# Kernel optimization log

Measured on AMD Instinct MI355X. Metric: run time of the kernel, lower is better.

The kernel has to match this reference:

```python
import jax, jax.numpy as jnp
import numpy as np

NT, NC = 100000, 25000
ETT, ECT = 800000, 400000
DIN_T, DIN_C = 64, 32
H, C = 4, 32
HID = H * C  # 128
SLOPE = 0.2  # GATConv LeakyReLU negative slope


def setup_inputs() -> dict:
    key = jax.random.key(0)
    ks = jax.random.split(key, 24)
    def p(i, shape, s=0.05):
        return jax.random.normal(ks[i], shape, dtype=jnp.float32) * s
    return {
        'x_target': jax.random.normal(ks[0], (NT, DIN_T), dtype=jnp.float32),
        'x_context': jax.random.normal(ks[1], (NC, DIN_C), dtype=jnp.float32),
        'edge_tt': jax.random.randint(ks[2], (2, ETT), 0, NT),
        'edge_ct_src': jax.random.randint(ks[3], (ECT,), 0, NC),
        'edge_ct_dst': jax.random.randint(ks[4], (ECT,), 0, NT),
        'W_pre_t': p(5, (DIN_T, HID)), 'b_pre_t': jnp.zeros((HID,), jnp.float32),
        'W_pre_c': p(6, (DIN_C, HID)), 'b_pre_c': jnp.zeros((HID,), jnp.float32),
        'W_sd': p(7, (HID, HID)), 'att_src_sd': p(8, (H, C)), 'att_dst_sd': p(9, (H, C)), 'b_sd': jnp.zeros((HID,), jnp.float32),
        'W_ds': p(10, (HID, HID)), 'att_src_ds': p(11, (H, C)), 'att_dst_ds': p(12, (H, C)), 'b_ds': jnp.zeros((HID,), jnp.float32),
        'W_ct_src': p(13, (HID, HID)), 'W_ct_dst': p(14, (HID, HID)), 'att_src_ct': p(15, (H, C)), 'att_dst_ct': p(16, (H, C)), 'b_ct': jnp.zeros((HID,), jnp.float32),
        'W_out': p(17, (HID, HID)), 'b_out': jnp.zeros((HID,), jnp.float32),
    }


def _gat(h_src, h_dst, att_s, att_d, src, dst, n_dst, bias):
    # h_src: [N_src,H,C] transformed src feats; h_dst: [N_dst,H,C]
    a_s = jnp.einsum('nhc,hc->nh', h_src, att_s)  # [N_src,H]
    a_d = jnp.einsum('nhc,hc->nh', h_dst, att_d)  # [N_dst,H]
    e = a_s[src] + a_d[dst]                        # [E,H]
    e = jnp.where(e > 0, e, SLOPE * e)             # LeakyReLU(0.2)
    m = jax.ops.segment_max(e, dst, num_segments=n_dst)  # stable softmax per dst
    ex = jnp.exp(e - m[dst])
    den = jax.ops.segment_sum(ex, dst, num_segments=n_dst)
    alpha = ex / den[dst]                          # [E,H]
    msg = h_src[src] * alpha[:, :, None]           # [E,H,C]
    out = jax.ops.segment_sum(msg, dst, num_segments=n_dst)
    return out.reshape(n_dst, H * C) + bias


def reference(x_target, x_context, edge_tt, edge_ct_src, edge_ct_dst,
              W_pre_t, b_pre_t, W_pre_c, b_pre_c,
              W_sd, att_src_sd, att_dst_sd, b_sd,
              W_ds, att_src_ds, att_dst_ds, b_ds,
              W_ct_src, W_ct_dst, att_src_ct, att_dst_ct, b_ct,
              W_out, b_out):
    # HeteroDictLinear pretransform + relu
    h_t = jax.nn.relu(x_target @ W_pre_t + b_pre_t)   # [NT,128]
    h_c = jax.nn.relu(x_context @ W_pre_c + b_pre_c)  # [NC,128]
    res = h_t
    # DirGATConv on (target,to,target): forward + reversed, each w/ self-loops
    loops = jnp.arange(NT)
    src_f = jnp.concatenate([edge_tt[0], loops]); dst_f = jnp.concatenate([edge_tt[1], loops])
    src_r = jnp.concatenate([edge_tt[1], loops]); dst_r = jnp.concatenate([edge_tt[0], loops])
    hs = (h_t @ W_sd).reshape(NT, H, C)
    out_sd = _gat(hs, hs, att_src_sd, att_dst_sd, src_f, dst_f, NT, b_sd)
    hd = (h_t @ W_ds).reshape(NT, H, C)
    out_ds = _gat(hd, hd, att_src_ds, att_dst_ds, src_r, dst_r, NT, b_ds)
    out_tt = 0.5 * out_sd + 0.5 * out_ds  # (1-alpha), alpha with alpha=0.5
    # bipartite GATConv on (context,to,target), no self loops
    hcs = (h_c @ W_ct_src).reshape(NC, H, C)
    htd = (h_t @ W_ct_dst).reshape(NT, H, C)
    out_ct = _gat(hcs, htd, att_src_ct, att_dst_ct, edge_ct_src, edge_ct_dst, NT, b_ct)
    # HeteroConv aggr='mean' over the two edge types hitting 'target'
    x = 0.5 * (out_tt + out_ct)
    x = jax.nn.relu(x + res)  # skip connection + relu
    return x @ W_out + b_out
```

## Files before the change

kernel.cpp:

```cpp
#include <hip/hip_runtime.h>
#include <cstdint>
#include <cstddef>

typedef unsigned short u16;
typedef unsigned int u32;

#define NT 100000
#define NC 25000
#define ETT 800000
#define ECT 400000
#define SLOPE 0.2f
#define OFFS (NT + 4)

#define NBK 782
#define NBLK 256
#define CHT ((ETT + NBLK - 1) / NBLK)
#define CHC ((ECT + NBLK - 1) / NBLK)
#define TOTC (3 * NBK * NBLK)
#define NSB ((TOTC + 2047) / 2048)

typedef __attribute__((ext_vector_type(8))) short bf16x8;
typedef __attribute__((ext_vector_type(4))) float f32x4;

__device__ __forceinline__ u16 f2bf(float f) {
  u32 u = __float_as_uint(f);
  u32 r = (u >> 16) & 1u;
  return (u16)((u + 0x7fffu + r) >> 16);
}
__device__ __forceinline__ float lof(u32 p) { return __uint_as_float(p << 16); }
__device__ __forceinline__ float hif(u32 p) { return __uint_as_float(p & 0xffff0000u); }

__global__ __launch_bounds__(256) void pre_t_kernel(const float* __restrict__ in,
    const float* __restrict__ W, const float* __restrict__ bias,
    const float* __restrict__ fold_cd, u16* __restrict__ h_t,
    float* __restrict__ aD, int N)
{
  __shared__ float s_in[32][33];
  __shared__ float s_W[32][128];
  __shared__ float s_fold[512];
  const int t = threadIdx.x;
  s_fold[t] = fold_cd[t];
  s_fold[t + 256] = fold_cd[t + 256];
  const int row0 = blockIdx.x * 32;
  const int rl = t >> 3, cg = t & 7;
  const int gr = row0 + rl;
  float acc[4][4];
  for (int g = 0; g < 4; ++g)
    for (int j = 0; j < 4; ++j)
      acc[g][j] = bias[g * 32 + cg * 4 + j];
  for (int kc = 0; kc < 64; kc += 32) {
    {
      float4 f = make_float4(0.f, 0.f, 0.f, 0.f);
      if (gr < N) f = *(const float4*)(in + (size_t)gr * 64 + kc + cg * 4);
      s_in[rl][cg * 4 + 0] = f.x; s_in[rl][cg * 4 + 1] = f.y;
      s_in[rl][cg * 4 + 2] = f.z; s_in[rl][cg * 4 + 3] = f.w;
    }
    for (int j = 0; j < 4; ++j) {
      const int idx = t + j * 256;
      const int k = idx >> 5, c4 = (idx & 31) * 4;
      *(float4*)&s_W[k][c4] = *(const float4*)(W + (size_t)(kc + k) * 128 + c4);
    }
    __syncthreads();
#pragma unroll 8
    for (int k = 0; k < 32; ++k) {
      const float a = s_in[rl][k];
      for (int g = 0; g < 4; ++g) {
        const float4 w = *(const float4*)&s_W[k][g * 32 + cg * 4];
        acc[g][0] = fmaf(a, w.x, acc[g][0]);
        acc[g][1] = fmaf(a, w.y, acc[g][1]);
        acc[g][2] = fmaf(a, w.z, acc[g][2]);
        acc[g][3] = fmaf(a, w.w, acc[g][3]);
      }
    }
    __syncthreads();
  }
  if (gr < N) {
    float p0 = 0.f, p1 = 0.f, p2 = 0.f, p3 = 0.f;
    for (int g = 0; g < 4; ++g) {
      for (int j = 0; j < 4; ++j) acc[g][j] = fmaxf(acc[g][j], 0.f);
      uint2 pk;
      pk.x = (u32)f2bf(acc[g][0]) | ((u32)f2bf(acc[g][1]) << 16);
      pk.y = (u32)f2bf(acc[g][2]) | ((u32)f2bf(acc[g][3]) << 16);
      *(uint2*)(h_t + (size_t)gr * 128 + g * 32 + cg * 4) = pk;
      for (int j = 0; j < 4; ++j) {
        const int col = g * 32 + cg * 4 + j;
        const float4 f4 = *(const float4*)&s_fold[col * 4];
        const float a = acc[g][j];
        p0 = fmaf(a, f4.x, p0); p1 = fmaf(a, f4.y, p1);
        p2 = fmaf(a, f4.z, p2); p3 = fmaf(a, f4.w, p3);
      }
    }
    for (int m = 1; m < 8; m <<= 1) {
      p0 += __shfl_xor(p0, m); p1 += __shfl_xor(p1, m);
      p2 += __shfl_xor(p2, m); p3 += __shfl_xor(p3, m);
    }
    if (cg == 0) *(float4*)(aD + (size_t)gr * 4) = make_float4(p0, p1, p2, p3);
  }
}

__global__ __launch_bounds__(256) void prep_kernel(
    const float* __restrict__ Wsd, const float* __restrict__ AsSd, const float* __restrict__ AdSd,
    const float* __restrict__ Wds, const float* __restrict__ AsDs, const float* __restrict__ AdDs,
    const float* __restrict__ Wout, u16* __restrict__ bf_sd, u16* __restrict__ bf_ds,
    u16* __restrict__ bf_out,
    const float* __restrict__ Wcd, const float* __restrict__ attD,
    const float* __restrict__ bsd, const float* __restrict__ bds, const float* __restrict__ bct,
    float* __restrict__ fold_cd, float* __restrict__ cbias)
{
  const int b = blockIdx.x;
  const int tid = threadIdx.x;
  if (b == 3) {
    if (tid < 128) {
      for (int h = 0; h < 4; ++h) {
        float s = 0.f;
        for (int c = 0; c < 32; ++c)
          s = fmaf(Wcd[tid * 128 + h * 32 + c], attD[h * 32 + c], s);
        fold_cd[tid * 4 + h] = s;
      }
      cbias[tid] = 0.25f * bsd[tid] + 0.25f * bds[tid] + 0.5f * bct[tid];
    }
    return;
  }
  __shared__ float fS[512], fD[512];
  const float* W = (b == 0) ? Wsd : (b == 1) ? Wds : Wout;
  const float* As = (b == 0) ? AsSd : AsDs;
  const float* Ad = (b == 0) ? AdSd : AdDs;
  u16* out = (b == 0) ? bf_sd : (b == 1) ? bf_ds : bf_out;
  const int tiles = (b == 2) ? 8 : 9;
  if (b < 2) {
    if (tid < 128) {
      for (int h = 0; h < 4; ++h) {
        float s1 = 0.f, s2 = 0.f;
        for (int c = 0; c < 32; ++c) {
          const float wv = W[tid * 128 + h * 32 + c];
          s1 = fmaf(wv, As[h * 32 + c], s1);
          s2 = fmaf(wv, Ad[h * 32 + c], s2);
        }
        fS[tid * 4 + h] = s1; fD[tid * 4 + h] = s2;
      }
    }
    __syncthreads();
  }
  const int total = tiles * 4 * 64 * 8;
  for (int i = tid; i < total; i += 256) {
    const int j = i & 7, lane = (i >> 3) & 63, ks = (i >> 9) & 3, t = i >> 11;
    const int k = ks * 32 + (lane >> 4) * 8 + j;
    const int n = t * 16 + (lane & 15);
    float v;
    if (n < 128) v = W[k * 128 + n];
    else if (n < 132) v = fS[k * 4 + (n - 128)];
    else if (n < 136) v = fD[k * 4 + (n - 132)];
    else v = 0.f;
    out[i] = f2bf(v);
  }
}

__global__ __launch_bounds__(256) void mfma_logits2_kernel(
    const short* __restrict__ A, const short* __restrict__ Bsd, const short* __restrict__ Bds,
    u16* __restrict__ hs, float* __restrict__ aSsd, float* __restrict__ aDsd,
    u16* __restrict__ hd, float* __restrict__ aSds, float* __restrict__ aDds, int M)
{
  __shared__ __align__(16) float lds[4][16][148];
  const int wv = threadIdx.x >> 6, lane = threadIdx.x & 63;
  const int quad = lane >> 4, l16 = lane & 15;
  const int row0 = blockIdx.x * 64 + wv * 16;
  const int arow = min(row0 + l16, M - 1);
  const short* ap = A + (size_t)arow * 128 + quad * 8;
  bf16x8 af[4];
  for (int ks = 0; ks < 4; ++ks) af[ks] = *(const bf16x8*)(ap + ks * 32);
  const int row = row0 + l16;
  const int idx = lane & 7, rr = lane >> 3;
  for (int pass = 0; pass < 2; ++pass) {
    const short* B = pass ? Bds : Bsd;
    u16* outb = pass ? hd : hs;
    float* aS = pass ? aSds : aSsd;
    float* aD = pass ? aDds : aDsd;
    f32x4 acc[9];
    for (int t = 0; t < 9; ++t) acc[t] = (f32x4){0.f, 0.f, 0.f, 0.f};
    for (int ks = 0; ks < 4; ++ks)
      for (int t = 0; t < 9; ++t) {
        const bf16x8 bf = *(const bf16x8*)(B + ((t * 4 + ks) * 64 + lane) * 8);
        acc[t] = __builtin_amdgcn_mfma_f32_16x16x32_bf16(af[ks], bf, acc[t], 0, 0, 0);
      }
    for (int t = 0; t < 9; ++t)
      for (int r = 0; r < 4; ++r)
        lds[wv][quad * 4 + r][t * 16 + l16] = acc[t][r];
    __syncthreads();
    if (row < M) {
      for (int g = 0; g < 8; ++g) {
        const f32x4 v = *(const f32x4*)&lds[wv][l16][g * 16 + quad * 4];
        uint2 pk;
        pk.x = (u32)f2bf(v[0]) | ((u32)f2bf(v[1]) << 16);
        pk.y = (u32)f2bf(v[2]) | ((u32)f2bf(v[3]) << 16);
        *(uint2*)(outb + (size_t)row * 128 + g * 16 + quad * 4) = pk;
      }
    }
    for (int p = 0; p < 2; ++p) {
      const int lr = p * 8 + rr;
      const int n = row0 + lr;
      if (n < M) {
        const float v = lds[wv][lr][128 + idx];
        if (idx < 4) aS[(size_t)n * 4 + idx] = v;
        else aD[(size_t)n * 4 + idx - 4] = v;
      }
    }
    __syncthreads();
  }
}

__global__ __launch_bounds__(256) void mfma_out_kernel(
    const short* __restrict__ A, const short* __restrict__ B,
    const float* __restrict__ bias, float* __restrict__ out, int M)
{
  __shared__ __align__(16) float lds[4][16][132];
  const int wv = threadIdx.x >> 6, lane = threadIdx.x & 63;
  const int quad = lane >> 4, l16 = lane & 15;
  const int row0 = blockIdx.x * 64 + wv * 16;
  const int arow = min(row0 + l16, M - 1);
  const short* ap = A + (size_t)arow * 128 + quad * 8;
  bf16x8 af[4];
  for (int ks = 0; ks < 4; ++ks) af[ks] = *(const bf16x8*)(ap + ks * 32);
  f32x4 acc[8];
  for (int t = 0; t < 8; ++t) acc[t] = (f32x4){0.f, 0.f, 0.f, 0.f};
  for (int ks = 0; ks < 4; ++ks)
    for (int t = 0; t < 8; ++t) {
      const bf16x8 bf = *(const bf16x8*)(B + ((t * 4 + ks) * 64 + lane) * 8);
      acc[t] = __builtin_amdgcn_mfma_f32_16x16x32_bf16(af[ks], bf, acc[t], 0, 0, 0);
    }
  for (int t = 0; t < 8; ++t)
    for (int r = 0; r < 4; ++r)
      lds[wv][quad * 4 + r][t * 16 + l16] = acc[t][r];
  __syncthreads();
  const int row = row0 + l16;
  if (row < M) {
    for (int g = 0; g < 8; ++g) {
      const int col = g * 16 + quad * 4;
      f32x4 v = *(const f32x4*)&lds[wv][l16][col];
      const f32x4 b4 = *(const f32x4*)(bias + col);
      v = v + b4;
      *(f32x4*)(out + (size_t)row * 128 + col) = v;
    }
  }
}

__global__ __launch_bounds__(256) void ctx_kernel(const float* __restrict__ x_c,
    const float* __restrict__ Wpc, const float* __restrict__ bpc,
    const float* __restrict__ Wcs, const float* __restrict__ attS,
    u16* __restrict__ hc_bf, float* __restrict__ aS, int N)
{
  __shared__ float s_in[32][33];
  __shared__ float s_W[32][128];
  __shared__ float s_h[32][132];
  const int t = threadIdx.x;
  const int row0 = blockIdx.x * 32;
  const int rl = t >> 3, cg = t & 7;
  const int gr = row0 + rl;
  {
    float4 f = make_float4(0.f, 0.f, 0.f, 0.f);
    if (gr < N) f = *(const float4*)(x_c + (size_t)gr * 32 + cg * 4);
    s_in[rl][cg * 4 + 0] = f.x; s_in[rl][cg * 4 + 1] = f.y;
    s_in[rl][cg * 4 + 2] = f.z; s_in[rl][cg * 4 + 3] = f.w;
  }
  for (int j = 0; j < 4; ++j) {
    const int idx = t + j * 256;
    const int k = idx >> 5, c4 = (idx & 31) * 4;
    *(float4*)&s_W[k][c4] = *(const float4*)(Wpc + (size_t)k * 128 + c4);
  }
  __syncthreads();
  float acc[4][4];
  for (int g = 0; g < 4; ++g)
    for (int j = 0; j < 4; ++j) acc[g][j] = bpc[g * 32 + cg * 4 + j];
#pragma unroll 8
  for (int k = 0; k < 32; ++k) {
    const float a = s_in[rl][k];
    for (int g = 0; g < 4; ++g) {
      const float4 w = *(const float4*)&s_W[k][g * 32 + cg * 4];
      acc[g][0] = fmaf(a, w.x, acc[g][0]);
      acc[g][1] = fmaf(a, w.y, acc[g][1]);
      acc[g][2] = fmaf(a, w.z, acc[g][2]);
      acc[g][3] = fmaf(a, w.w, acc[g][3]);
    }
  }
  for (int g = 0; g < 4; ++g)
    *(float4*)&s_h[rl][g * 32 + cg * 4] =
        make_float4(fmaxf(acc[g][0], 0.f), fmaxf(acc[g][1], 0.f),
                    fmaxf(acc[g][2], 0.f), fmaxf(acc[g][3], 0.f));
  __syncthreads();
  float acc2[4][4];
  for (int g = 0; g < 4; ++g)
    for (int j = 0; j < 4; ++j) acc2[g][j] = 0.f;
  for (int kc = 0; kc < 128; kc += 32) {
    for (int j = 0; j < 4; ++j) {
      const int idx = t + j * 256;
      const int k = idx >> 5, c4 = (idx & 31) * 4;
      *(float4*)&s_W[k][c4] = *(const float4*)(Wcs + (size_t)(kc + k) * 128 + c4);
    }
    __syncthreads();
#pragma unroll 8
    for (int k = 0; k < 32; ++k) {
      const float a = s_h[rl][kc + k];
      for (int g = 0; g < 4; ++g) {
        const float4 w = *(const float4*)&s_W[k][g * 32 + cg * 4];
        acc2[g][0] = fmaf(a, w.x, acc2[g][0]);
        acc2[g][1] = fmaf(a, w.y, acc2[g][1]);
        acc2[g][2] = fmaf(a, w.z, acc2[g][2]);
        acc2[g][3] = fmaf(a, w.w, acc2[g][3]);
      }
    }
    __syncthreads();
  }
  if (gr < N) {
    float pS[4];
    for (int g = 0; g < 4; ++g) {
      uint2 pk;
      pk.x = (u32)f2bf(acc2[g][0]) | ((u32)f2bf(acc2[g][1]) << 16);
      pk.y = (u32)f2bf(acc2[g][2]) | ((u32)f2bf(acc2[g][3]) << 16);
      *(uint2*)(hc_bf + (size_t)gr * 128 + g * 32 + cg * 4) = pk;
      const float4 as4 = *(const float4*)(attS + g * 32 + cg * 4);
      pS[g] = acc2[g][0] * as4.x + acc2[g][1] * as4.y + acc2[g][2] * as4.z + acc2[g][3] * as4.w;
    }
    for (int m = 1; m < 8; m <<= 1)
      for (int g = 0; g < 4; ++g) pS[g] += __shfl_xor(pS[g], m);
    if (cg == 0)
      *(float4*)(aS + (size_t)gr * 4) = make_float4(pS[0], pS[1], pS[2], pS[3]);
  }
}

__global__ __launch_bounds__(256) void hist_blk_kernel(const int* __restrict__ tt_src,
    const int* __restrict__ tt_dst, const int* __restrict__ ect_d, int* __restrict__ cntblk)
{
  __shared__ int h[3 * NBK];
  const int t = threadIdx.x, b = blockIdx.x;
  for (int i = t; i < 3 * NBK; i += 256) h[i] = 0;
  __syncthreads();
  const int lo = b * CHT, hi = min(lo + CHT, ETT);
  for (int i = lo + t; i < hi; i += 256) {
    atomicAdd(&h[tt_dst[i] >> 7], 1);
    atomicAdd(&h[NBK + (tt_src[i] >> 7)], 1);
  }
  const int lo2 = b * CHC, hi2 = min(lo2 + CHC, ECT);
  for (int i = lo2 + t; i < hi2; i += 256)
    atomicAdd(&h[2 * NBK + (ect_d[i] >> 7)], 1);
  __syncthreads();
  for (int i = t; i < 3 * NBK; i += 256)
    cntblk[(size_t)i * NBLK + b] = h[i];
}

__global__ __launch_bounds__(256) void scan2_blk_kernel(const int* __restrict__ in,
    int* __restrict__ out, int* __restrict__ bsum)
{
  const int t = threadIdx.x, b = blockIdx.x;
  const int idx = b * 2048 + t * 8;
  int v[8];
  int s = 0;
  if (idx < TOTC) {
    const int4 q0 = *(const int4*)(in + idx);
    const int4 q1 = *(const int4*)(in + idx + 4);
    int x;
    x = q0.x; v[0] = s; s += x;  x = q0.y; v[1] = s; s += x;
    x = q0.z; v[2] = s; s += x;  x = q0.w; v[3] = s; s += x;
    x = q1.x; v[4] = s; s += x;  x = q1.y; v[5] = s; s += x;
    x = q1.z; v[6] = s; s += x;  x = q1.w; v[7] = s; s += x;
  } else {
    for (int j = 0; j < 8; ++j) v[j] = 0;
  }
  __shared__ int sh[256];
  sh[t] = s;
  __syncthreads();
  for (int d = 1; d < 256; d <<= 1) {
    const int u = (t >= d) ? sh[t - d] : 0;
    __syncthreads();
    sh[t] += u;
    __syncthreads();
  }
  const int excl = (t == 0) ? 0 : sh[t - 1];
  if (idx < TOTC) {
    int4 q0, q1;
    q0.x = excl + v[0]; q0.y = excl + v[1]; q0.z = excl + v[2]; q0.w = excl + v[3];
    q1.x = excl + v[4]; q1.y = excl + v[5]; q1.z = excl + v[6]; q1.w = excl + v[7];
    *(int4*)(out + idx) = q0;
    *(int4*)(out + idx + 4) = q1;
  }
  if (t == 255) bsum[b] = sh[255];
}

__global__ __launch_bounds__(512) void scan2_top_kernel(const int* __restrict__ bsum,
    int* __restrict__ bpre)
{
  __shared__ int sh[512];
  const int t = threadIdx.x;
  const int orig = (t < NSB) ? bsum[t] : 0;
  sh[t] = orig;
  __syncthreads();
  for (int d = 1; d < 512; d <<= 1) {
    const int v = (t >= d) ? sh[t - d] : 0;
    __syncthreads();
    sh[t] += v;
    __syncthreads();
  }
  if (t < NSB) bpre[t] = sh[t] - orig;
}

__global__ __launch_bounds__(256) void scan2_add_kernel(const int* __restrict__ bpre,
    int* __restrict__ out)
{
  const int t = threadIdx.x, b = blockIdx.x;
  const int bp = bpre[b];
  const int idx = b * 2048 + t * 8;
  if (idx < TOTC) {
    int4 q0 = *(const int4*)(out + idx);
    int4 q1 = *(const int4*)(out + idx + 4);
    q0.x += bp; q0.y += bp; q0.z += bp; q0.w += bp;
    q1.x += bp; q1.y += bp; q1.z += bp; q1.w += bp;
    *(int4*)(out + idx) = q0;
    *(int4*)(out + idx + 4) = q1;
  }
}

__global__ __launch_bounds__(256) void bin_kernel(const int* __restrict__ tt_src,
    const int* __restrict__ tt_dst, const int* __restrict__ ect_s, const int* __restrict__ ect_d,
    const int* __restrict__ scanned, u32* __restrict__ bin)
{
  __shared__ int cur[3 * NBK];
  const int t = threadIdx.x, b = blockIdx.x;
  for (int i = t; i < 3 * NBK; i += 256)
    cur[i] = scanned[(size_t)i * NBLK + b];
  __syncthreads();
  const int lo = b * CHT, hi = min(lo + CHT, ETT);
  for (int i = lo + t; i < hi; i += 256) {
    const int s = tt_src[i], d = tt_dst[i];
    int p = atomicAdd(&cur[d >> 7], 1);
    bin[p] = ((u32)(d & 127) << 17) | (u32)s;
    p = atomicAdd(&cur[NBK + (s >> 7)], 1);
    bin[p] = ((u32)(s & 127) << 17) | (u32)d;
  }
  const int lo2 = b * CHC, hi2 = min(lo2 + CHC, ECT);
  for (int i = lo2 + t; i < hi2; i += 256) {
    const int s = ect_s[i], d = ect_d[i];
    const int p = atomicAdd(&cur[2 * NBK + (d >> 7)], 1);
    bin[p] = ((u32)(d & 127) << 17) | (u32)s;
  }
}

__global__ __launch_bounds__(256) void bucket_fill_kernel(const int* __restrict__ scanned,
    const u32* __restrict__ bin, int* __restrict__ offs, int* __restrict__ big_el)
{
  const int rel = blockIdx.x / NBK;
  const int bucket = blockIdx.x - rel * NBK;
  const int t = threadIdx.x;
  __shared__ int s_cnt[128], s_exc[128], s_cur[128];
  if (t < 128) s_cnt[t] = 0;
  __syncthreads();
  const int base = scanned[(size_t)blockIdx.x * NBLK];
  const int nxt = (blockIdx.x == 3 * NBK - 1) ? (2 * ETT + ECT)
                                              : scanned[((size_t)blockIdx.x + 1) * NBLK];
  const int size = nxt - base;
  for (int i = t; i < size; i += 256)
    atomicAdd(&s_cnt[bin[base + i] >> 17], 1);
  __syncthreads();
  if (t < 128) s_exc[t] = s_cnt[t];
  __syncthreads();
  for (int d = 1; d < 128; d <<= 1) {
    int v = 0;
    if (t < 128 && t >= d) v = s_exc[t - d];
    __syncthreads();
    if (t < 128) s_exc[t] += v;
    __syncthreads();
  }
  const int relbase = rel * ETT;
  const int obase = base - relbase;
  int* off_rel = offs + (size_t)rel * OFFS;
  const int node0 = bucket * 128;
  if (t < 128) {
    const int excl = s_exc[t] - s_cnt[t];
    s_cur[t] = obase + excl;
    if (node0 + t < NT) off_rel[node0 + t] = obase + excl;
  }
  if (t == 0 && bucket == NBK - 1) off_rel[NT] = obase + size;
  __syncthreads();
  int* el_rel = big_el + relbase;
  for (int i = t; i < size; i += 256) {
    const u32 e = bin[base + i];
    const int pos = atomicAdd(&s_cur[e >> 17], 1);
    el_rel[pos] = (int)(e & 0x1FFFFu);
  }
}

__device__ __forceinline__ void gat_pipe16(const int* __restrict__ off,
    const int* __restrict__ el, const float* __restrict__ aS, const float* __restrict__ aD,
    const u16* __restrict__ hb, int d, int h, int cb, int self_loop, float w,
    float* __restrict__ acc)
{
  const float ad = aD[(size_t)d * 4 + h];
  const int beg = off[d];
  const int m = off[d + 1] - beg;
  const int cnt = m + self_loop;
  if (cnt <= 0) return;
  float den = 0.f;
  float a0 = 0.f, a1 = 0.f, a2 = 0.f, a3 = 0.f, a4 = 0.f, a5 = 0.f, a6 = 0.f, a7 = 0.f;
  int sB = (1 < m) ? el[beg + 1] : d;
  {
    const int sA0 = (0 < m) ? el[beg] : d;
    float eA = aS[(size_t)sA0 * 4 + h];
    uint4 pA = *(const uint4*)(hb + (size_t)sA0 * 128 + cb);
    for (int k = 0; k < cnt; ++k) {
      const int sC = (k + 2 < m) ? el[beg + k + 2] : d;
      const float eB = aS[(size_t)sB * 4 + h];
      const uint4 pB = *(const uint4*)(hb + (size_t)sB * 128 + cb);
      float ea = eA + ad;
      ea = ea > 0.f ? ea : SLOPE * ea;
      const float ex = __expf(ea);
      den += ex;
      a0 = fmaf(ex, lof(pA.x), a0); a1 = fmaf(ex, hif(pA.x), a1);
      a2 = fmaf(ex, lof(pA.y), a2); a3 = fmaf(ex, hif(pA.y), a3);
      a4 = fmaf(ex, lof(pA.z), a4); a5 = fmaf(ex, hif(pA.z), a5);
      a6 = fmaf(ex, lof(pA.w), a6); a7 = fmaf(ex, hif(pA.w), a7);
      eA = eB; pA = pB; sB = sC;
    }
  }
  const float s = w / den;
  acc[0] = fmaf(a0, s, acc[0]); acc[1] = fmaf(a1, s, acc[1]);
  acc[2] = fmaf(a2, s, acc[2]); acc[3] = fmaf(a3, s, acc[3]);
  acc[4] = fmaf(a4, s, acc[4]); acc[5] = fmaf(a5, s, acc[5]);
  acc[6] = fmaf(a6, s, acc[6]); acc[7] = fmaf(a7, s, acc[7]);
}

__global__ __launch_bounds__(256) void gather_all_kernel(
    const int* __restrict__ off_f, const int* __restrict__ el_f,
    const float* __restrict__ aS_sd, const float* __restrict__ aD_sd, const u16* __restrict__ hs,
    const int* __restrict__ off_r, const int* __restrict__ el_r,
    const float* __restrict__ aS_ds, const float* __restrict__ aD_ds, const u16* __restrict__ hd,
    const int* __restrict__ off_c, const int* __restrict__ el_c,
    const float* __restrict__ aS_ct, const float* __restrict__ aD_ct, const u16* __restrict__ hc,
    const u16* __restrict__ skip, const float* __restrict__ cbias, u16* __restrict__ x)
{
  const int d = blockIdx.x * 16 + (threadIdx.x >> 4);
  if (d >= NT) return;
  const int lg = threadIdx.x & 15;
  const int h = lg >> 2;
  const int cb = lg * 8;
  float acc[8];
  for (int i = 0; i < 8; ++i) acc[i] = 0.f;
  gat_pipe16(off_f, el_f, aS_sd, aD_sd, hs, d, h, cb, 1, 0.25f, acc);
  gat_pipe16(off_r, el_r, aS_ds, aD_ds, hd, d, h, cb, 1, 0.25f, acc);
  gat_pipe16(off_c, el_c, aS_ct, aD_ct, hc, d, h, cb, 0, 0.5f, acc);
  const uint4 sk = *(const uint4*)(skip + (size_t)d * 128 + cb);
  const float4 cb0 = *(const float4*)(cbias + cb);
  const float4 cb1 = *(const float4*)(cbias + cb + 4);
  const float o0 = fmaxf(acc[0] + cb0.x + lof(sk.x), 0.f);
  const float o1 = fmaxf(acc[1] + cb0.y + hif(sk.x), 0.f);
  const float o2 = fmaxf(acc[2] + cb0.z + lof(sk.y), 0.f);
  const float o3 = fmaxf(acc[3] + cb0.w + hif(sk.y), 0.f);
  const float o4 = fmaxf(acc[4] + cb1.x + lof(sk.z), 0.f);
  const float o5 = fmaxf(acc[5] + cb1.y + hif(sk.z), 0.f);
  const float o6 = fmaxf(acc[6] + cb1.z + lof(sk.w), 0.f);
  const float o7 = fmaxf(acc[7] + cb1.w + hif(sk.w), 0.f);
  uint4 r;
  r.x = (u32)f2bf(o0) | ((u32)f2bf(o1) << 16);
  r.y = (u32)f2bf(o2) | ((u32)f2bf(o3) << 16);
  r.z = (u32)f2bf(o4) | ((u32)f2bf(o5) << 16);
  r.w = (u32)f2bf(o6) | ((u32)f2bf(o7) << 16);
  *(uint4*)(x + (size_t)d * 128 + cb) = r;
}

extern "C" void kernel_launch(void* const* d_in, const int* in_sizes, int n_in,
                              void* d_out, int out_size, void* d_ws, size_t ws_size,
                              hipStream_t stream)
{
  const float* x_t   = (const float*)d_in[0];
  const float* x_c   = (const float*)d_in[1];
  const int*   e_tt  = (const int*)d_in[2];
  const int*   ect_s = (const int*)d_in[3];
  const int*   ect_d = (const int*)d_in[4];
  const float* Wpt = (const float*)d_in[5];   const float* bpt = (const float*)d_in[6];
  const float* Wpc = (const float*)d_in[7];   const float* bpc = (const float*)d_in[8];
  const float* Wsd = (const float*)d_in[9];   const float* As_sd = (const float*)d_in[10];
  const float* Ad_sd = (const float*)d_in[11]; const float* bsd = (const float*)d_in[12];
  const float* Wds = (const float*)d_in[13];  const float* As_ds = (const float*)d_in[14];
  const float* Ad_ds = (const float*)d_in[15]; const float* bds = (const float*)d_in[16];
  const float* Wcs = (const float*)d_in[17];  const float* Wcd = (const float*)d_in[18];
  const float* As_ct = (const float*)d_in[19]; const float* Ad_ct = (const float*)d_in[20];
  const float* bct = (const float*)d_in[21];
  const float* Wout = (const float*)d_in[22]; const float* bout = (const float*)d_in[23];

  char* p = (char*)d_ws;
  size_t off = 0;
  auto alloc = [&](size_t bytes) { char* r = p + off; off += (bytes + 255) & ~(size_t)255; return r; };
  u16* ht_bf   = (u16*)alloc((size_t)NT * 128 * 2);
  u16* hs_bf   = (u16*)alloc((size_t)NT * 128 * 2);
  u16* hd_bf   = (u16*)alloc((size_t)NT * 128 * 2);
  u16* hc_bf   = (u16*)alloc((size_t)NC * 128 * 2);
  u16* x_bf    = (u16*)alloc((size_t)NT * 128 * 2);
  float* aS_sd = (float*)alloc((size_t)NT * 4 * 4);
  float* aD_sd = (float*)alloc((size_t)NT * 4 * 4);
  float* aS_ds = (float*)alloc((size_t)NT * 4 * 4);
  float* aD_ds = (float*)alloc((size_t)NT * 4 * 4);
  float* aS_ct = (float*)alloc((size_t)NC * 4 * 4);
  float* aD_ct = (float*)alloc((size_t)NT * 4 * 4);
  int* cntblk  = (int*)alloc((size_t)TOTC * 4);
  int* scanned = (int*)alloc((size_t)TOTC * 4);
  u32* bin     = (u32*)alloc((size_t)(2 * ETT + ECT) * 4);
  int* big_el  = (int*)alloc((size_t)(2 * ETT + ECT) * 4);
  int* offs    = (int*)alloc((size_t)3 * OFFS * 4);
  int* bsum    = (int*)alloc((size_t)NSB * 4);
  int* bpre    = (int*)alloc((size_t)NSB * 4);
  float* fold_cd = (float*)alloc(512 * 4);
  float* cbias   = (float*)alloc(128 * 4);
  u16* bfrag_sd  = (u16*)alloc((size_t)9 * 4 * 64 * 8 * 2);
  u16* bfrag_ds  = (u16*)alloc((size_t)9 * 4 * 64 * 8 * 2);
  u16* bfrag_out = (u16*)alloc((size_t)8 * 4 * 64 * 8 * 2);

  int* off_f = offs;
  int* off_r = offs + OFFS;
  int* off_c = offs + 2 * OFFS;
  int* el_f = big_el;
  int* el_r = big_el + ETT;
  int* el_c = big_el + 2 * ETT;

  const int* tt_src = e_tt;
  const int* tt_dst = e_tt + ETT;

  const int gT = (NT + 31) / 32;
  const int gC = (NC + 31) / 32;
  const int gM = (NT + 63) / 64;

  hist_blk_kernel<<<NBLK, 256, 0, stream>>>(tt_src, tt_dst, ect_d, cntblk);
  scan2_blk_kernel<<<NSB, 256, 0, stream>>>(cntblk, scanned, bsum);
  scan2_top_kernel<<<1, 512, 0, stream>>>(bsum, bpre);
  scan2_add_kernel<<<NSB, 256, 0, stream>>>(bpre, scanned);
  bin_kernel<<<NBLK, 256, 0, stream>>>(tt_src, tt_dst, ect_s, ect_d, scanned, bin);
  bucket_fill_kernel<<<3 * NBK, 256, 0, stream>>>(scanned, bin, offs, big_el);

  prep_kernel<<<4, 256, 0, stream>>>(Wsd, As_sd, Ad_sd, Wds, As_ds, Ad_ds, Wout,
                                     bfrag_sd, bfrag_ds, bfrag_out,
                                     Wcd, Ad_ct, bsd, bds, bct, fold_cd, cbias);

  pre_t_kernel<<<gT, 256, 0, stream>>>(x_t, Wpt, bpt, fold_cd, ht_bf, aD_ct, NT);
  mfma_logits2_kernel<<<gM, 256, 0, stream>>>((const short*)ht_bf,
      (const short*)bfrag_sd, (const short*)bfrag_ds,
      hs_bf, aS_sd, aD_sd, hd_bf, aS_ds, aD_ds, NT);
  ctx_kernel<<<gC, 256, 0, stream>>>(x_c, Wpc, bpc, Wcs, As_ct, hc_bf, aS_ct, NC);

  gather_all_kernel<<<(NT + 15) / 16, 256, 0, stream>>>(
      off_f, el_f, aS_sd, aD_sd, hs_bf,
      off_r, el_r, aS_ds, aD_ds, hd_bf,
      off_c, el_c, aS_ct, aD_ct, hc_bf,
      ht_bf, cbias, x_bf);

  mfma_out_kernel<<<gM, 256, 0, stream>>>((const short*)x_bf, (const short*)bfrag_out,
                                          bout, (float*)d_out, NT);
}
```

Baseline: 441.8 us.

## Deepen gather pipeline to four edges per step and fold log2e into attention scores

The per-destination GAT gather loop now processes four edges per iteration and keeps two pairs of loads plus four prefetched edge indices in flight, where before it prefetched only one edge ahead. This targets the latency of dependent random gathers. The attention projections are pre-scaled by log2(e) so the loop can call exp2f directly, and address math is done in 32-bit with uint4 indexing. The cost is more registers per thread, which may lower occupancy, plus some wasted loads of the self-loop row at the tail of each list.

```diff
diff --git a/kernel.cpp b/kernel.cpp
--- a/kernel.cpp
+++ b/kernel.cpp
@@ -10,6 +10,7 @@
 #define ETT 800000
 #define ECT 400000
 #define SLOPE 0.2f
+#define LOG2E 1.4426950408889634f
 #define OFFS (NT + 4)
 
 #define NBK 782
@@ -115,7 +116,7 @@
         float s = 0.f;
         for (int c = 0; c < 32; ++c)
           s = fmaf(Wcd[tid * 128 + h * 32 + c], attD[h * 32 + c], s);
-        fold_cd[tid * 4 + h] = s;
+        fold_cd[tid * 4 + h] = s * LOG2E;
       }
       cbias[tid] = 0.25f * bsd[tid] + 0.25f * bds[tid] + 0.5f * bct[tid];
     }
@@ -136,7 +137,7 @@
           s1 = fmaf(wv, As[h * 32 + c], s1);
           s2 = fmaf(wv, Ad[h * 32 + c], s2);
         }
-        fS[tid * 4 + h] = s1; fD[tid * 4 + h] = s2;
+        fS[tid * 4 + h] = s1 * LOG2E; fD[tid * 4 + h] = s2 * LOG2E;
       }
     }
     __syncthreads();
@@ -322,7 +323,8 @@
     for (int m = 1; m < 8; m <<= 1)
       for (int g = 0; g < 4; ++g) pS[g] += __shfl_xor(pS[g], m);
     if (cg == 0)
-      *(float4*)(aS + (size_t)gr * 4) = make_float4(pS[0], pS[1], pS[2], pS[3]);
+      *(float4*)(aS + (size_t)gr * 4) =
+          make_float4(pS[0] * LOG2E, pS[1] * LOG2E, pS[2] * LOG2E, pS[3] * LOG2E);
   }
 }
 
@@ -486,43 +488,81 @@
   }
 }
 
+__device__ __forceinline__ void acc8(float ex, uint4 p, float* __restrict__ a) {
+  a[0] = fmaf(ex, lof(p.x), a[0]); a[1] = fmaf(ex, hif(p.x), a[1]);
+  a[2] = fmaf(ex, lof(p.y), a[2]); a[3] = fmaf(ex, hif(p.y), a[3]);
+  a[4] = fmaf(ex, lof(p.z), a[4]); a[5] = fmaf(ex, hif(p.z), a[5]);
+  a[6] = fmaf(ex, lof(p.w), a[6]); a[7] = fmaf(ex, hif(p.w), a[7]);
+}
+
 __device__ __forceinline__ void gat_pipe16(const int* __restrict__ off,
     const int* __restrict__ el, const float* __restrict__ aS, const float* __restrict__ aD,
-    const u16* __restrict__ hb, int d, int h, int cb, int self_loop, float w,
+    const u16* __restrict__ hb, int d, int h, int lg, int self_loop, float w,
     float* __restrict__ acc)
 {
-  const float ad = aD[(size_t)d * 4 + h];
   const int beg = off[d];
   const int m = off[d + 1] - beg;
   const int cnt = m + self_loop;
   if (cnt <= 0) return;
+  const float ad = aD[(u32)d * 4u + (u32)h];
+  const uint4* __restrict__ hb4 = (const uint4*)hb;
+  const u32 lgo = (u32)lg;
   float den = 0.f;
-  float a0 = 0.f, a1 = 0.f, a2 = 0.f, a3 = 0.f, a4 = 0.f, a5 = 0.f, a6 = 0.f, a7 = 0.f;
-  int sB = (1 < m) ? el[beg + 1] : d;
-  {
-    const int sA0 = (0 < m) ? el[beg] : d;
-    float eA = aS[(size_t)sA0 * 4 + h];
-    uint4 pA = *(const uint4*)(hb + (size_t)sA0 * 128 + cb);
-    for (int k = 0; k < cnt; ++k) {
-      const int sC = (k + 2 < m) ? el[beg + k + 2] : d;
-      const float eB = aS[(size_t)sB * 4 + h];
-      const uint4 pB = *(const uint4*)(hb + (size_t)sB * 128 + cb);
-      float ea = eA + ad;
-      ea = ea > 0.f ? ea : SLOPE * ea;
-      const float ex = __expf(ea);
-      den += ex;
-      a0 = fmaf(ex, lof(pA.x), a0); a1 = fmaf(ex, hif(pA.x), a1);
-      a2 = fmaf(ex, lof(pA.y), a2); a3 = fmaf(ex, hif(pA.y), a3);
-      a4 = fmaf(ex, lof(pA.z), a4); a5 = fmaf(ex, hif(pA.z), a5);
-      a6 = fmaf(ex, lof(pA.w), a6); a7 = fmaf(ex, hif(pA.w), a7);
-      eA = eB; pA = pB; sB = sC;
-    }
+  float a[8];
+#pragma unroll
+  for (int i = 0; i < 8; ++i) a[i] = 0.f;
+  const int sA0 = (0 < m) ? el[beg + 0] : d;
+  const int sA1 = (1 < m) ? el[beg + 1] : d;
+  const int sB0 = (2 < m) ? el[beg + 2] : d;
+  const int sB1 = (3 < m) ? el[beg + 3] : d;
+  float eA0 = aS[(u32)sA0 * 4u + (u32)h];
+  float eA1 = aS[(u32)sA1 * 4u + (u32)h];
+  uint4 pA0 = hb4[(u32)sA0 * 16u + lgo];
+  uint4 pA1 = hb4[(u32)sA1 * 16u + lgo];
+  float eB0 = aS[(u32)sB0 * 4u + (u32)h];
+  float eB1 = aS[(u32)sB1 * 4u + (u32)h];
+  uint4 pB0 = hb4[(u32)sB0 * 16u + lgo];
+  uint4 pB1 = hb4[(u32)sB1 * 16u + lgo];
+  int tp0 = (4 < m) ? el[beg + 4] : d;
+  int tp1 = (5 < m) ? el[beg + 5] : d;
+  int tp2 = (6 < m) ? el[beg + 6] : d;
+  int tp3 = (7 < m) ? el[beg + 7] : d;
+#pragma unroll 1
+  for (int k = 0; k < cnt; k += 4) {
+    {
+      float x0 = eA0 + ad; x0 = fmaxf(x0, SLOPE * x0);
+      float x1 = eA1 + ad; x1 = fmaxf(x1, SLOPE * x1);
+      const float ex0 = exp2f(x0);
+      const float ex1 = (k + 1 < cnt) ? exp2f(x1) : 0.f;
+      den += ex0 + ex1;
+      acc8(ex0, pA0, a);
+      acc8(ex1, pA1, a);
+    }
+    eA0 = aS[(u32)tp0 * 4u + (u32)h];
+    eA1 = aS[(u32)tp1 * 4u + (u32)h];
+    pA0 = hb4[(u32)tp0 * 16u + lgo];
+    pA1 = hb4[(u32)tp1 * 16u + lgo];
+    {
+      float x0 = eB0 + ad; x0 = fmaxf(x0, SLOPE * x0);
+      float x1 = eB1 + ad; x1 = fmaxf(x1, SLOPE * x1);
+      const float ex0 = (k + 2 < cnt) ? exp2f(x0) : 0.f;
+      const float ex1 = (k + 3 < cnt) ? exp2f(x1) : 0.f;
+      den += ex0 + ex1;
+      acc8(ex0, pB0, a);
+      acc8(ex1, pB1, a);
+    }
+    eB0 = aS[(u32)tp2 * 4u + (u32)h];
+    eB1 = aS[(u32)tp3 * 4u + (u32)h];
+    pB0 = hb4[(u32)tp2 * 16u + lgo];
+    pB1 = hb4[(u32)tp3 * 16u + lgo];
+    tp0 = (k + 8 < m) ? el[beg + k + 8] : d;
+    tp1 = (k + 9 < m) ? el[beg + k + 9] : d;
+    tp2 = (k + 10 < m) ? el[beg + k + 10] : d;
+    tp3 = (k + 11 < m) ? el[beg + k + 11] : d;
   }
   const float s = w / den;
-  acc[0] = fmaf(a0, s, acc[0]); acc[1] = fmaf(a1, s, acc[1]);
-  acc[2] = fmaf(a2, s, acc[2]); acc[3] = fmaf(a3, s, acc[3]);
-  acc[4] = fmaf(a4, s, acc[4]); acc[5] = fmaf(a5, s, acc[5]);
-  acc[6] = fmaf(a6, s, acc[6]); acc[7] = fmaf(a7, s, acc[7]);
+#pragma unroll
+  for (int i = 0; i < 8; ++i) acc[i] = fmaf(a[i], s, acc[i]);
 }
 
 __global__ __launch_bounds__(256) void gather_all_kernel(
@@ -541,9 +581,9 @@
   const int cb = lg * 8;
   float acc[8];
   for (int i = 0; i < 8; ++i) acc[i] = 0.f;
-  gat_pipe16(off_f, el_f, aS_sd, aD_sd, hs, d, h, cb, 1, 0.25f, acc);
-  gat_pipe16(off_r, el_r, aS_ds, aD_ds, hd, d, h, cb, 1, 0.25f, acc);
-  gat_pipe16(off_c, el_c, aS_ct, aD_ct, hc, d, h, cb, 0, 0.5f, acc);
+  gat_pipe16(off_f, el_f, aS_sd, aD_sd, hs, d, h, lg, 1, 0.25f, acc);
+  gat_pipe16(off_r, el_r, aS_ds, aD_ds, hd, d, h, lg, 1, 0.25f, acc);
+  gat_pipe16(off_c, el_c, aS_ct, aD_ct, hc, d, h, lg, 0, 0.5f, acc);
   const uint4 sk = *(const uint4*)(skip + (size_t)d * 128 + cb);
   const float4 cb0 = *(const float4*)(cbias + cb);
   const float4 cb1 = *(const float4*)(cbias + cb + 4);
```

New measurement: 445.0 us. Within noise of the previous version (+0.7%).
